# Optimization experiments

Hardware: AMD Instinct MI355X
Metric: run time of the kernel (lower is better)

## Reference

```python
import jax, jax.numpy as jnp
import numpy as np
from jax import lax

# ---- config constants (mirror init_kwargs) ----
PC_MIN_X, PC_MIN_Y, PC_MIN_Z = 0.0, -40.0, -3.0
PC_MAX_X, PC_MAX_Y, PC_MAX_Z = 70.4, 40.0, 1.0
VX, VY = 0.05, 0.05
NUM_KEYPOINTS = 2048
RADII = (0.4, 0.8)
NSAMPLE = (16, 16)
EPS = 1e-5


def setup_inputs() -> dict:
    key = jax.random.key(0)
    ks = jax.random.split(key, 16)
    B, N = 2, 32768
    u = jax.random.uniform(ks[0], (B, N, 4), dtype=jnp.float32)
    x = u[..., 0] * (PC_MAX_X - PC_MIN_X) + PC_MIN_X
    y = u[..., 1] * (PC_MAX_Y - PC_MIN_Y) + PC_MIN_Y
    z = u[..., 2] * (PC_MAX_Z - PC_MIN_Z) + PC_MIN_Z
    points = jnp.stack([x, y, z, u[..., 3]], axis=-1)  # (B,N,4): xyz + intensity
    spatial_features = jax.random.normal(ks[1], (B, 256, 200, 176), dtype=jnp.float32)
    p = lambda k, s: jax.random.normal(k, s, dtype=jnp.float32) * 0.1
    return dict(
        points=points, spatial_features=spatial_features,
        w0_0=p(ks[2], (4, 16)), g0_0=jnp.ones(16), b0_0=jnp.zeros(16),
        w0_1=p(ks[3], (16, 16)), g0_1=jnp.ones(16), b0_1=jnp.zeros(16),
        w1_0=p(ks[4], (4, 16)), g1_0=jnp.ones(16), b1_0=jnp.zeros(16),
        w1_1=p(ks[5], (16, 16)), g1_1=jnp.ones(16), b1_1=jnp.zeros(16),
        wf=p(ks[6], (288, 128)), gf=jnp.ones(128), bf=jnp.zeros(128),
        bev_stride=8,
    )


def _bn(x, g, b, axes):
    m = jnp.mean(x, axis=axes, keepdims=True)
    v = jnp.var(x, axis=axes, keepdims=True)
    return (x - m) * lax.rsqrt(v + EPS) * g + b


def _fps(xyz, K):
    # farthest point sampling, pointnet2 semantics (start at index 0)
    B, N, _ = xyz.shape
    def step(carry, _):
        dists, last = carry
        p = jax.vmap(lambda a, i: a[i])(xyz, last)           # (B,3)
        d = jnp.sum((xyz - p[:, None, :]) ** 2, axis=-1)     # (B,N)
        dists = jnp.minimum(dists, d)
        nxt = jnp.argmax(dists, axis=-1).astype(jnp.int32)
        return (dists, nxt), nxt
    init = (jnp.full((B, N), 1e10, xyz.dtype), jnp.zeros((B,), jnp.int32))
    _, rest = lax.scan(step, init, None, length=K - 1)       # (K-1,B)
    return jnp.concatenate([jnp.zeros((B, 1), jnp.int32), rest.T], axis=1)  # (B,K)


def _ball_group_pool(pts, kp, dist2, radius, ns, layers):
    # pts: (B,N,4) xyz+feat, kp: (B,K,3), dist2: (B,K,N) (stop-grad)
    B, N = pts.shape[0], pts.shape[1]
    valid = dist2 < radius * radius
    score = jnp.where(valid, -jnp.arange(N, dtype=jnp.float32), -jnp.inf)
    vals, idx = lax.top_k(score, ns)                          # first ns in-radius indices
    ok = jnp.isfinite(vals)                                   # (B,K,ns)
    idx = jnp.where(ok, idx, idx[..., :1])                    # duplicate first valid
    empty = ~ok[..., 0]                                       # (B,K) no neighbor at all
    grouped = jax.vmap(lambda p, i: p[i])(pts, idx)           # (B,K,ns,4)
    rel = grouped[..., :3] - kp[:, :, None, :]
    h = jnp.concatenate([rel, grouped[..., 3:]], axis=-1)     # (B,K,ns,4)
    h = jnp.where(empty[..., None, None], 0.0, h)
    for w, g, b in layers:
        h = jax.nn.relu(_bn(h @ w, g, b, axes=(0, 1, 2)))
    pooled = jnp.max(h, axis=2)                               # (B,K,C)
    return jnp.where(empty[..., None], 0.0, pooled)


def _bev_interp(kp, bev, stride):
    # kp: (B,K,3), bev: (B,C,H,W); torch bilinear_interpolate semantics
    B, C, H, W = bev.shape
    xi = (kp[..., 0] - PC_MIN_X) / VX / stride                # (B,K)
    yi = (kp[..., 1] - PC_MIN_Y) / VY / stride
    x0 = jnp.clip(jnp.floor(xi).astype(jnp.int32), 0, W - 1)
    x1 = jnp.clip(jnp.floor(xi).astype(jnp.int32) + 1, 0, W - 1)
    y0 = jnp.clip(jnp.floor(yi).astype(jnp.int32), 0, H - 1)
    y1 = jnp.clip(jnp.floor(yi).astype(jnp.int32) + 1, 0, H - 1)
    gat = jax.vmap(lambda f, yy, xx: f[:, yy, xx].T)          # (K,C) per batch
    Ia, Ib = gat(bev, y0, x0), gat(bev, y1, x0)
    Ic, Id = gat(bev, y0, x1), gat(bev, y1, x1)
    x0f, x1f = x0.astype(jnp.float32), x1.astype(jnp.float32)
    y0f, y1f = y0.astype(jnp.float32), y1.astype(jnp.float32)
    wa = ((x1f - xi) * (y1f - yi))[..., None]
    wb = ((x1f - xi) * (yi - y0f))[..., None]
    wc = ((xi - x0f) * (y1f - yi))[..., None]
    wd = ((xi - x0f) * (yi - y0f))[..., None]
    return Ia * wa + Ib * wb + Ic * wc + Id * wd              # (B,K,C)


def reference(points, spatial_features, w0_0, g0_0, b0_0, w0_1, g0_1, b0_1,
              w1_0, g1_0, b1_0, w1_1, g1_1, b1_1, wf, gf, bf, bev_stride):
    xyz = points[..., :3]                                     # (B,N,3)
    idx = _fps(xyz, NUM_KEYPOINTS)                            # (B,K)
    kp = jax.vmap(lambda p, i: p[i])(xyz, idx)                # keypoints (B,K,3)

    # BEV bilinear interpolation
    bev_feats = _bev_interp(kp, spatial_features, bev_stride) # (B,K,256)

    # raw-points multi-scale ball-query aggregation
    dist2 = lax.stop_gradient(
        jnp.sum((kp[:, :, None, :] - xyz[:, None, :, :]) ** 2, axis=-1))  # (B,K,N)
    p0 = _ball_group_pool(points, kp, dist2, RADII[0], NSAMPLE[0],
                          [(w0_0, g0_0, b0_0), (w0_1, g0_1, b0_1)])
    p1 = _ball_group_pool(points, kp, dist2, RADII[1], NSAMPLE[1],
                          [(w1_0, g1_0, b1_0), (w1_1, g1_1, b1_1)])

    feat = jnp.concatenate([bev_feats, p0, p1], axis=-1)      # (B,K,288)
    M = feat.shape[0] * feat.shape[1]
    feat = feat.reshape(M, -1)
    h = feat @ wf                                             # Linear no bias
    h = _bn(h, gf, bf, axes=(0,))                             # BatchNorm1d (train mode)
    return jax.nn.relu(h)                                     # (M,128)
```

## Files before the change

kernel.cpp:

```cpp
#include <hip/hip_runtime.h>
#include <hip/hip_bf16.h>
#include <limits.h>
#include <cstddef>

#define B_SZ    2
#define N_PTS   32768
#define N_KP    2048
#define N_CHUNK 512
#define H_BEV   200
#define W_BEV   176
#define C_BEV   256
#define FEAT_DIM 288
#define C_OUT   128
#define M_ROWS  4096

__device__ __forceinline__ float sqd(float ax, float ay, float az,
                                     float bx, float by, float bz) {
  float dx = ax - bx, dy = ay - by, dz = az - bz;
  return __fadd_rn(__fadd_rn(dx * dx, dy * dy), dz * dz);
}

__device__ __forceinline__ unsigned part1by1(unsigned n) {
  n &= 0xFFFF;
  n = (n | (n << 8)) & 0x00FF00FF;
  n = (n | (n << 4)) & 0x0F0F0F0F;
  n = (n | (n << 2)) & 0x33333333;
  n = (n | (n << 1)) & 0x55555555;
  return n;
}

__global__ void cell_count(const float4* __restrict__ pts,
                           int* __restrict__ codes, int* __restrict__ counts) {
  const int b = blockIdx.x, tid = threadIdx.x;
  __shared__ int cnt[4096];
  for (int k = tid; k < 4096; k += 1024) cnt[k] = 0;
  __syncthreads();
  for (int j = 0; j < 32; ++j) {
    int i = j * 1024 + tid;
    float4 v = pts[(size_t)b * N_PTS + i];
    int cx = min(63, max(0, (int)(v.x * (64.0f / 70.4f))));
    int cy = min(63, max(0, (int)((v.y + 40.0f) * 0.8f)));
    int code = (int)(part1by1((unsigned)cx) | (part1by1((unsigned)cy) << 1));
    codes[(size_t)b * N_PTS + i] = code;
    atomicAdd(&cnt[code], 1);
  }
  __syncthreads();
  for (int k = tid; k < 4096; k += 1024) counts[b * 4096 + k] = cnt[k];
}

__global__ void cell_scan(const int* __restrict__ counts, int* __restrict__ offs) {
  const int b = blockIdx.x, lane = threadIdx.x;
  const int* cnt = counts + b * 4096;
  int* off = offs + b * 4096;
  int s = 0;
  for (int k = 0; k < 64; ++k) s += cnt[lane * 64 + k];
  int incl = s;
#pragma unroll
  for (int o = 1; o < 64; o <<= 1) {
    int t = __shfl_up(incl, o);
    if (lane >= o) incl += t;
  }
  int run = incl - s;
  for (int k = 0; k < 64; ++k) {
    int id = lane * 64 + k;
    int t = cnt[id];
    off[id] = run;
    run += t;
  }
}

__global__ void scatter_pts(const float4* __restrict__ pts,
                            const int* __restrict__ codes,
                            int* __restrict__ offs,
                            float4* __restrict__ spts, int* __restrict__ sorig) {
  const int b = blockIdx.x, tid = threadIdx.x;
  for (int j = 0; j < 32; ++j) {
    int i = j * 1024 + tid;
    int code = codes[(size_t)b * N_PTS + i];
    int pos = atomicAdd(&offs[b * 4096 + code], 1);
    spts[(size_t)b * N_PTS + pos] = pts[(size_t)b * N_PTS + i];
    sorig[(size_t)b * N_PTS + pos] = i;
  }
}

__global__ void chunk_bbox(const float4* __restrict__ spts, float* __restrict__ bbox) {
  const int wid = threadIdx.x >> 6, lane = threadIdx.x & 63;
  const int chunk = blockIdx.x * 4 + wid;
  const int b = chunk >> 9, c = chunk & (N_CHUNK - 1);
  float4 v = spts[(size_t)b * N_PTS + c * 64 + lane];
  float lx = v.x, ly = v.y, lz = v.z, hx = v.x, hy = v.y, hz = v.z;
#pragma unroll
  for (int o = 32; o >= 1; o >>= 1) {
    lx = fminf(lx, __shfl_xor(lx, o)); hx = fmaxf(hx, __shfl_xor(hx, o));
    ly = fminf(ly, __shfl_xor(ly, o)); hy = fmaxf(hy, __shfl_xor(hy, o));
    lz = fminf(lz, __shfl_xor(lz, o)); hz = fmaxf(hz, __shfl_xor(hz, o));
  }
  if (lane == 0) {
    float* bp = bbox + (size_t)chunk * 6;
    bp[0] = lx; bp[1] = ly; bp[2] = lz; bp[3] = hx; bp[4] = hy; bp[5] = hz;
  }
}

__global__ void fps_pruned(const float4* __restrict__ pts,
                           const float4* __restrict__ spts,
                           const int* __restrict__ sorig,
                           const float* __restrict__ bbox,
                           float4* __restrict__ kp_xyz) {
  const int b = blockIdx.x;
  const int tid = threadIdx.x;
  const int wid = tid >> 6, lane = tid & 63;
  const float4* p4o = pts + (size_t)b * N_PTS;
  const float4* sp4 = spts + (size_t)b * N_PTS;
  const int* sog = sorig + (size_t)b * N_PTS;

  __shared__ float d_lds[N_PTS];
  __shared__ float bb[N_CHUNK * 6];
  __shared__ float keyd[N_CHUNK];
  __shared__ int keyo[N_CHUNK];
  __shared__ int dirty_s[N_CHUNK];
  __shared__ unsigned long long wkey[8];
  __shared__ float sxs, sys, szs;
  __shared__ int ndirty_s;

  for (int i = tid; i < N_PTS; i += 1024) d_lds[i] = 1e10f;
  for (int i = tid; i < N_CHUNK * 6; i += 1024) bb[i] = bbox[(size_t)b * N_CHUNK * 6 + i];
  if (tid < N_CHUNK) { keyd[tid] = 1e10f; keyo[tid] = 0; }
  if (tid == 0) {
    float4 p0 = p4o[0];
    kp_xyz[b * N_KP] = p0;
    sxs = p0.x; sys = p0.y; szs = p0.z;
    ndirty_s = 0;
  }
  __syncthreads();

  for (int it = 1; it < N_KP; ++it) {
    const float sx = sxs, sy = sys, sz = szs;
    if (tid < N_CHUNK) {
      const float* bp = bb + tid * 6;
      float dxm = fmaxf(fmaxf(bp[0] - sx, sx - bp[3]), 0.f);
      float dym = fmaxf(fmaxf(bp[1] - sy, sy - bp[4]), 0.f);
      float dzm = fmaxf(fmaxf(bp[2] - sz, sz - bp[5]), 0.f);
      float lb = (dxm * dxm + dym * dym) + dzm * dzm;
      if (lb * 0.99999f < keyd[tid]) {
        int p = atomicAdd(&ndirty_s, 1);
        dirty_s[p] = tid;
      }
    }
    __syncthreads();
    const int K = ndirty_s;
    for (int r = 0; r * 16 < K; ++r) {
      int ci = r * 16 + wid;
      if (ci < K) {
        int c = dirty_s[ci];
        int i = (c << 6) + lane;
        float4 sp = sp4[i];
        float ss = sqd(sp.x, sp.y, sp.z, sx, sy, sz);
        float nd = fminf(d_lds[i], ss);
        d_lds[i] = nd;
        float m = nd;
#pragma unroll
        for (int o = 32; o >= 1; o >>= 1) m = fmaxf(m, __shfl_xor(m, o));
        int og = sog[i];
        int cand = (nd == m) ? og : INT_MAX;
#pragma unroll
        for (int o = 32; o >= 1; o >>= 1) cand = min(cand, __shfl_xor(cand, o));
        if (lane == 0) { keyd[c] = m; keyo[c] = cand; }
      }
    }
    __syncthreads();
    if (tid < N_CHUNK) {
      unsigned long long key =
          ((unsigned long long)__float_as_uint(keyd[tid]) << 32) |
          (unsigned long long)(0xFFFFFFFFu - (unsigned)keyo[tid]);
#pragma unroll
      for (int o = 32; o >= 1; o >>= 1) {
        unsigned long long t = __shfl_xor(key, o);
        key = (t > key) ? t : key;
      }
      if (lane == 0) wkey[wid] = key;
    }
    __syncthreads();
    if (tid == 0) {
      unsigned long long k = wkey[0];
#pragma unroll
      for (int w = 1; w < 8; ++w) k = (wkey[w] > k) ? wkey[w] : k;
      int worig = (int)(0xFFFFFFFFu - (unsigned)(k & 0xFFFFFFFFu));
      float4 wp = p4o[worig];
      kp_xyz[b * N_KP + it] = wp;
      sxs = wp.x; sys = wp.y; szs = wp.z;
      ndirty_s = 0;
    }
    __syncthreads();
  }
}

__global__ void bev_kernel(const float4* __restrict__ kp,
                           const float* __restrict__ bev,
                           const int* __restrict__ stride_p,
                           float* __restrict__ feat) {
  const int kpi = blockIdx.x;
  const int c = threadIdx.x;
  const int b = kpi >> 11;
  float4 k = kp[kpi];
  float sf = (float)stride_p[0];
  float xi = (k.x - 0.0f) / 0.05f / sf;
  float yi = (k.y - (-40.0f)) / 0.05f / sf;
  int fx = (int)floorf(xi), fy = (int)floorf(yi);
  int x0 = min(max(fx, 0), W_BEV - 1), x1 = min(max(fx + 1, 0), W_BEV - 1);
  int y0 = min(max(fy, 0), H_BEV - 1), y1 = min(max(fy + 1, 0), H_BEV - 1);
  float x0f = (float)x0, x1f = (float)x1, y0f = (float)y0, y1f = (float)y1;
  float wa = (x1f - xi) * (y1f - yi);
  float wb = (x1f - xi) * (yi - y0f);
  float wc = (xi - x0f) * (y1f - yi);
  float wd = (xi - x0f) * (yi - y0f);
  const float* fb = bev + (size_t)b * C_BEV * (H_BEV * W_BEV) + (size_t)c * (H_BEV * W_BEV);
  float Ia = fb[y0 * W_BEV + x0], Ib = fb[y1 * W_BEV + x0];
  float Ic = fb[y0 * W_BEV + x1], Id = fb[y1 * W_BEV + x1];
  feat[(size_t)kpi * FEAT_DIM + c] = ((Ia * wa + Ib * wb) + Ic * wc) + Id * wd;
}

__device__ __forceinline__ int sel4(int q, int a, int b, int c, int d) {
  return q == 0 ? a : (q == 1 ? b : (q == 2 ? c : d));
}

__global__ void ballq_kernel(const float4* __restrict__ pts,
                             const float4* __restrict__ kp,
                             int* __restrict__ lists,
                             int* __restrict__ cnts) {
  const int w = threadIdx.x >> 6;
  const int lane = threadIdx.x & 63;
  const int kpbase = blockIdx.x * 16 + w * 4;
  const int b = blockIdx.x >> 7;
  const float4* p4 = pts + (size_t)b * N_PTS;
  __shared__ int l0[4][4][16];
  __shared__ int l1[4][4][16];
  float kx[4], ky[4], kz[4];
  int c0[4] = {0, 0, 0, 0}, c1[4] = {0, 0, 0, 0};
#pragma unroll
  for (int q = 0; q < 4; ++q) {
    float4 kq = kp[kpbase + q];
    kx[q] = kq.x; ky[q] = kq.y; kz[q] = kq.z;
  }
  const float R0SQ = (float)(0.4 * 0.4);
  const float R1SQ = (float)(0.8 * 0.8);
  const unsigned long long below = (lane == 0) ? 0ull : ((~0ull) >> (64 - lane));

  for (int r = 0; r < N_PTS / 64; ++r) {
    const int i = r * 64 + lane;
    float4 v = p4[i];
#pragma unroll
    for (int q = 0; q < 4; ++q) {
      float dd = sqd(v.x, v.y, v.z, kx[q], ky[q], kz[q]);
      bool in1 = dd < R1SQ;
      unsigned long long m1 = __ballot(in1);
      if (m1) {
        bool in0 = dd < R0SQ;
        unsigned long long m0 = __ballot(in0);
        if (c0[q] < 16) {
          if (in0) { int pos = c0[q] + __popcll(m0 & below); if (pos < 16) l0[w][q][pos] = i; }
          c0[q] += __popcll(m0);
        }
        if (c1[q] < 16) {
          if (in1) { int pos = c1[q] + __popcll(m1 & below); if (pos < 16) l1[w][q][pos] = i; }
          c1[q] += __popcll(m1);
        }
      }
    }
  }
  int q = lane >> 4, s = lane & 15;
  int kpi = kpbase + q;
  int cA = sel4(q, min(c0[0], 16), min(c0[1], 16), min(c0[2], 16), min(c0[3], 16));
  int cB = sel4(q, min(c1[0], 16), min(c1[1], 16), min(c1[2], 16), min(c1[3], 16));
  int vA = (s < cA) ? l0[w][q][s] : (cA > 0 ? l0[w][q][0] : 0);
  int vB = (s < cB) ? l1[w][q][s] : (cB > 0 ? l1[w][q][0] : 0);
  lists[(size_t)(0 * M_ROWS + kpi) * 16 + s] = vA;
  lists[(size_t)(1 * M_ROWS + kpi) * 16 + s] = vB;
  if (lane < 4) {
    cnts[0 * M_ROWS + kpbase + lane] = sel4(lane, min(c0[0], 16), min(c0[1], 16), min(c0[2], 16), min(c0[3], 16));
    cnts[1 * M_ROWS + kpbase + lane] = sel4(lane, min(c1[0], 16), min(c1[1], 16), min(c1[2], 16), min(c1[3], 16));
  }
}

__global__ void group_mlp1(const float4* __restrict__ pts,
                           const float4* __restrict__ kp,
                           const int* __restrict__ lists,
                           const int* __restrict__ cnts,
                           const float* __restrict__ w00,
                           const float* __restrict__ w10,
                           float* __restrict__ abuf) {
  int gid = blockIdx.x * 256 + threadIdx.x;
  int br = gid >> 16;
  int rem = gid & 65535;
  int bkp = rem >> 4, s = rem & 15;
  int b = bkp >> 11;
  __shared__ float wl[64];
  if (threadIdx.x < 64) wl[threadIdx.x] = (br ? w10 : w00)[threadIdx.x];
  __syncthreads();
  int cnt = cnts[br * M_ROWS + bkp];
  float h0 = 0.f, h1 = 0.f, h2 = 0.f, h3 = 0.f;
  if (cnt > 0) {
    int pidx = lists[(size_t)(br * M_ROWS + bkp) * 16 + s];
    float4 p = pts[(size_t)b * N_PTS + pidx];
    float4 k = kp[bkp];
    h0 = p.x - k.x; h1 = p.y - k.y; h2 = p.z - k.z; h3 = p.w;
  }
  float* out = abuf + (size_t)gid * 16;
#pragma unroll
  for (int c = 0; c < 16; ++c)
    out[c] = ((h0 * wl[c] + h1 * wl[16 + c]) + h2 * wl[32 + c]) + h3 * wl[48 + c];
}

__global__ void stats16_partial(const float* __restrict__ a, float* __restrict__ part) {
  int br = blockIdx.y, bl = blockIdx.x, t = threadIdx.x;
  const float* base = a + (size_t)br * 65536 * 16;
  float s[16], q[16];
#pragma unroll
  for (int c = 0; c < 16; ++c) { s[c] = 0.f; q[c] = 0.f; }
  for (int rr = 0; rr < 4; ++rr) {
    int row = bl * 1024 + rr * 256 + t;
#pragma unroll
    for (int c = 0; c < 16; ++c) {
      float v = base[(size_t)row * 16 + c];
      s[c] += v; q[c] += v * v;
    }
  }
  __shared__ float sbs[256][16];
  __shared__ float sbq[256][16];
#pragma unroll
  for (int c = 0; c < 16; ++c) { sbs[t][c] = s[c]; sbq[t][c] = q[c]; }
  __syncthreads();
  for (int st = 128; st > 0; st >>= 1) {
    if (t < st) {
#pragma unroll
      for (int c = 0; c < 16; ++c) { sbs[t][c] += sbs[t + st][c]; sbq[t][c] += sbq[t + st][c]; }
    }
    __syncthreads();
  }
  if (t < 16) {
    part[(size_t)(br * 64 + bl) * 32 + t] = sbs[0][t];
    part[(size_t)(br * 64 + bl) * 32 + 16 + t] = sbq[0][t];
  }
}

__global__ void stats16_final(const float* __restrict__ part, float* __restrict__ stats) {
  int t = threadIdx.x;
  if (t < 32) {
    int br = t >> 4, c = t & 15;
    float s = 0.f, q = 0.f;
    for (int bl = 0; bl < 64; ++bl) {
      s += part[(size_t)(br * 64 + bl) * 32 + c];
      q += part[(size_t)(br * 64 + bl) * 32 + 16 + c];
    }
    float m = s / 65536.f;
    float var = q / 65536.f - m * m;
    stats[(br * 16 + c) * 2] = m;
    stats[(br * 16 + c) * 2 + 1] = rsqrtf(var + 1e-5f);
  }
}

__global__ void mlp2_kernel(float* __restrict__ abuf, const float* __restrict__ stats,
                            const float* __restrict__ g00, const float* __restrict__ b00,
                            const float* __restrict__ g10, const float* __restrict__ b10,
                            const float* __restrict__ w01, const float* __restrict__ w11) {
  int gid = blockIdx.x * 256 + threadIdx.x;
  int br = gid >> 16;
  __shared__ float wl[256];
  wl[threadIdx.x] = (br ? w11 : w01)[threadIdx.x];
  __syncthreads();
  const float* g = br ? g10 : g00;
  const float* bb = br ? b10 : b00;
  float* row = abuf + (size_t)gid * 16;
  float z[16];
#pragma unroll
  for (int f = 0; f < 16; ++f) {
    float m = stats[(br * 16 + f) * 2], is = stats[(br * 16 + f) * 2 + 1];
    z[f] = fmaxf(0.f, (row[f] - m) * is * g[f] + bb[f]);
  }
  float o[16];
#pragma unroll
  for (int c = 0; c < 16; ++c) o[c] = 0.f;
#pragma unroll
  for (int f = 0; f < 16; ++f) {
#pragma unroll
    for (int c = 0; c < 16; ++c) o[c] += z[f] * wl[f * 16 + c];
  }
#pragma unroll
  for (int c = 0; c < 16; ++c) row[c] = o[c];
}

__global__ void pool_kernel(const float* __restrict__ abuf, const float* __restrict__ stats,
                            const int* __restrict__ cnts,
                            const float* __restrict__ g01, const float* __restrict__ b01,
                            const float* __restrict__ g11, const float* __restrict__ b11,
                            float* __restrict__ feat) {
  int gid = blockIdx.x * 256 + threadIdx.x;
  int br = gid >> 16;
  int rem = gid & 65535;
  int bkp = rem >> 4, c = rem & 15;
  const float* g = br ? g11 : g01;
  const float* bb = br ? b11 : b01;
  float m = stats[(br * 16 + c) * 2], is = stats[(br * 16 + c) * 2 + 1];
  float gg = g[c], bv = bb[c];
  const float* base = abuf + ((size_t)br * 65536 + (size_t)bkp * 16) * 16 + c;
  float mx = -1e30f;
#pragma unroll
  for (int s = 0; s < 16; ++s) {
    float v = base[(size_t)s * 16];
    mx = fmaxf(mx, fmaxf(0.f, (v - m) * is * gg + bv));
  }
  if (cnts[br * M_ROWS + bkp] == 0) mx = 0.f;
  feat[(size_t)bkp * FEAT_DIM + 256 + br * 16 + c] = mx;
}

__global__ void final_mm(const float* __restrict__ feat, const float* __restrict__ wf,
                         float* __restrict__ hbuf) {
  int row = blockIdx.x;
  int c = threadIdx.x;
  __shared__ float fr[FEAT_DIM];
  for (int k = c; k < FEAT_DIM; k += 128) fr[k] = feat[(size_t)row * FEAT_DIM + k];
  __syncthreads();
  float acc = 0.f;
#pragma unroll 8
  for (int k = 0; k < FEAT_DIM; ++k) acc += fr[k] * wf[(size_t)k * C_OUT + c];
  hbuf[(size_t)row * C_OUT + c] = acc;
}

__global__ void stats128_partial(const float* __restrict__ hbuf, float* __restrict__ part) {
  int bl = blockIdx.x, c = threadIdx.x;
  float s = 0.f, q = 0.f;
  for (int r = 0; r < 128; ++r) {
    float v = hbuf[(size_t)(bl * 128 + r) * C_OUT + c];
    s += v; q += v * v;
  }
  part[(size_t)(bl * 128 + c) * 2] = s;
  part[(size_t)(bl * 128 + c) * 2 + 1] = q;
}

__global__ void stats128_final(const float* __restrict__ part, float* __restrict__ stats) {
  int c = threadIdx.x;
  float s = 0.f, q = 0.f;
  for (int bl = 0; bl < 32; ++bl) {
    s += part[(size_t)(bl * 128 + c) * 2];
    q += part[(size_t)(bl * 128 + c) * 2 + 1];
  }
  float m = s / 4096.f;
  float var = q / 4096.f - m * m;
  stats[c * 2] = m;
  stats[c * 2 + 1] = rsqrtf(var + 1e-5f);
}

__global__ void out_kernel(const float* __restrict__ hbuf, const float* __restrict__ stats,
                           const float* __restrict__ gf, const float* __restrict__ bf,
                           float* __restrict__ out) {
  int gid = blockIdx.x * 256 + threadIdx.x;
  int c = gid & 127;
  float v = hbuf[gid];
  float r = fmaxf(0.f, (v - stats[c * 2]) * stats[c * 2 + 1] * gf[c] + bf[c]);
  out[gid] = r;
}

extern "C" void kernel_launch(void* const* d_in, const int* in_sizes, int n_in,
                              void* d_out, int out_size, void* d_ws, size_t ws_size,
                              hipStream_t stream) {
  const float4* pts = (const float4*)d_in[0];
  const float* spatial = (const float*)d_in[1];
  const float* w0_0 = (const float*)d_in[2];
  const float* g0_0 = (const float*)d_in[3];
  const float* b0_0 = (const float*)d_in[4];
  const float* w0_1 = (const float*)d_in[5];
  const float* g0_1 = (const float*)d_in[6];
  const float* b0_1 = (const float*)d_in[7];
  const float* w1_0 = (const float*)d_in[8];
  const float* g1_0 = (const float*)d_in[9];
  const float* b1_0 = (const float*)d_in[10];
  const float* w1_1 = (const float*)d_in[11];
  const float* g1_1 = (const float*)d_in[12];
  const float* b1_1 = (const float*)d_in[13];
  const float* wf  = (const float*)d_in[14];
  const float* gf  = (const float*)d_in[15];
  const float* bfp = (const float*)d_in[16];
  const int* stride_p = (const int*)d_in[17];

  char* ws = (char*)d_ws;
  float4* kp_xyz = (float4*)(ws + 0);
  int* lists     = (int*)(ws + 65536);
  int* cnts      = (int*)(ws + 589824);
  float* abuf    = (float*)(ws + 622592);
  float* feat    = (float*)(ws + 9011200);
  float* hbuf    = (float*)(ws + 13729792);
  float* part16  = (float*)(ws + 15826944);
  float* stats16 = (float*)(ws + 15843328);
  float* part128 = (float*)(ws + 15843584);
  float* stats128= (float*)(ws + 15876352);

  char* sbase = (char*)abuf;
  float4* spts = (float4*)(sbase + 0);
  int* sorig   = (int*)(sbase + 1048576);
  int* codes   = (int*)(sbase + 1310720);
  int* counts  = (int*)(sbase + 1572864);
  int* offs    = (int*)(sbase + 1605632);
  float* bboxg = (float*)(sbase + 1638400);

  cell_count<<<B_SZ, 1024, 0, stream>>>(pts, codes, counts);
  cell_scan<<<B_SZ, 64, 0, stream>>>(counts, offs);
  scatter_pts<<<B_SZ, 1024, 0, stream>>>(pts, codes, offs, spts, sorig);
  chunk_bbox<<<256, 256, 0, stream>>>(spts, bboxg);
  fps_pruned<<<B_SZ, 1024, 0, stream>>>(pts, spts, sorig, bboxg, kp_xyz);
  bev_kernel<<<M_ROWS, 256, 0, stream>>>(kp_xyz, spatial, stride_p, feat);
  ballq_kernel<<<256, 256, 0, stream>>>(pts, kp_xyz, lists, cnts);
  group_mlp1<<<512, 256, 0, stream>>>(pts, kp_xyz, lists, cnts, w0_0, w1_0, abuf);
  stats16_partial<<<dim3(64, 2), 256, 0, stream>>>(abuf, part16);
  stats16_final<<<1, 64, 0, stream>>>(part16, stats16);
  mlp2_kernel<<<512, 256, 0, stream>>>(abuf, stats16, g0_0, b0_0, g1_0, b1_0, w0_1, w1_1);
  stats16_partial<<<dim3(64, 2), 256, 0, stream>>>(abuf, part16);
  stats16_final<<<1, 64, 0, stream>>>(part16, stats16);
  pool_kernel<<<512, 256, 0, stream>>>(abuf, stats16, cnts, g0_1, b0_1, g1_1, b1_1, feat);
  final_mm<<<M_ROWS, 128, 0, stream>>>(feat, wf, hbuf);
  stats128_partial<<<32, 128, 0, stream>>>(hbuf, part128);
  stats128_final<<<1, 128, 0, stream>>>(part128, stats128);
  out_kernel<<<2048, 256, 0, stream>>>(hbuf, stats128, gf, bfp, (float*)d_out);
}
```

Baseline: 4.060 ms.

## Cut FPS per-iteration barriers and global loads with redundant winner selection

The FPS loop now has every thread compute the final argmax from per-wave keys and read the winning point's xyz from LDS copies kept per chunk. This removes the serial thread-0 step, one __syncthreads, and a dependent global load of the winner each iteration. The dirty-chunk list is double-buffered so its counter can be reset without an extra barrier. Bounding boxes move from LDS into registers, and the first two chunk loads per wave are issued up front for more memory parallelism. The cost is extra LDS writes of xyz for each chunk max and a w=0 in the output keypoints instead of the original intensity.

Result: slower. 4.371 ms (+7.7%).

```diff
diff --git a/kernel.cpp b/kernel.cpp
--- a/kernel.cpp
+++ b/kernel.cpp
@@ -114,57 +114,90 @@
   const int* sog = sorig + (size_t)b * N_PTS;
 
   __shared__ float d_lds[N_PTS];
-  __shared__ float bb[N_CHUNK * 6];
   __shared__ float keyd[N_CHUNK];
   __shared__ int keyo[N_CHUNK];
-  __shared__ int dirty_s[N_CHUNK];
+  __shared__ float keyx[N_CHUNK];
+  __shared__ float keyy[N_CHUNK];
+  __shared__ float keyz[N_CHUNK];
+  __shared__ int dirty_s[2][N_CHUNK];
   __shared__ unsigned long long wkey[8];
-  __shared__ float sxs, sys, szs;
-  __shared__ int ndirty_s;
+  __shared__ int wchunk[8];
+  __shared__ int ndirty_s[2];
 
   for (int i = tid; i < N_PTS; i += 1024) d_lds[i] = 1e10f;
-  for (int i = tid; i < N_CHUNK * 6; i += 1024) bb[i] = bbox[(size_t)b * N_CHUNK * 6 + i];
-  if (tid < N_CHUNK) { keyd[tid] = 1e10f; keyo[tid] = 0; }
-  if (tid == 0) {
-    float4 p0 = p4o[0];
-    kp_xyz[b * N_KP] = p0;
-    sxs = p0.x; sys = p0.y; szs = p0.z;
-    ndirty_s = 0;
-  }
-  __syncthreads();
+  if (tid < N_CHUNK) keyd[tid] = 1e10f;
+  if (tid < 2) ndirty_s[tid] = 0;
+  float bx0 = 0.f, by0 = 0.f, bz0 = 0.f, bx1 = 0.f, by1 = 0.f, bz1 = 0.f;
+  if (tid < N_CHUNK) {
+    const float* bp = bbox + (size_t)b * N_CHUNK * 6 + (size_t)tid * 6;
+    bx0 = bp[0]; by0 = bp[1]; bz0 = bp[2]; bx1 = bp[3]; by1 = bp[4]; bz1 = bp[5];
+  }
+  float4 p0 = p4o[0];
+  float sx = p0.x, sy = p0.y, sz = p0.z;
+  if (tid == 0) kp_xyz[b * N_KP] = make_float4(sx, sy, sz, 0.f);
+  __syncthreads();
+
+#define PROC_CHUNK(cc, pp, og, dp)                                            \
+  {                                                                           \
+    float ss = sqd((pp).x, (pp).y, (pp).z, sx, sy, sz);                       \
+    float nd = fminf((dp), ss);                                               \
+    d_lds[((cc) << 6) + lane] = nd;                                           \
+    float mm = nd;                                                            \
+    _Pragma("unroll")                                                         \
+    for (int oo = 32; oo >= 1; oo >>= 1) mm = fmaxf(mm, __shfl_xor(mm, oo));  \
+    int cnd = (nd == mm) ? (og) : INT_MAX;                                    \
+    _Pragma("unroll")                                                         \
+    for (int oo = 32; oo >= 1; oo >>= 1) cnd = min(cnd, __shfl_xor(cnd, oo)); \
+    if ((og) == cnd) {                                                        \
+      keyd[cc] = mm; keyo[cc] = cnd;                                          \
+      keyx[cc] = (pp).x; keyy[cc] = (pp).y; keyz[cc] = (pp).z;                \
+    }                                                                         \
+  }
 
   for (int it = 1; it < N_KP; ++it) {
-    const float sx = sxs, sy = sys, sz = szs;
+    const int s = it & 1;
     if (tid < N_CHUNK) {
-      const float* bp = bb + tid * 6;
-      float dxm = fmaxf(fmaxf(bp[0] - sx, sx - bp[3]), 0.f);
-      float dym = fmaxf(fmaxf(bp[1] - sy, sy - bp[4]), 0.f);
-      float dzm = fmaxf(fmaxf(bp[2] - sz, sz - bp[5]), 0.f);
+      float dxm = fmaxf(fmaxf(bx0 - sx, sx - bx1), 0.f);
+      float dym = fmaxf(fmaxf(by0 - sy, sy - by1), 0.f);
+      float dzm = fmaxf(fmaxf(bz0 - sz, sz - bz1), 0.f);
       float lb = (dxm * dxm + dym * dym) + dzm * dzm;
       if (lb * 0.99999f < keyd[tid]) {
-        int p = atomicAdd(&ndirty_s, 1);
-        dirty_s[p] = tid;
+        int p = atomicAdd(&ndirty_s[s], 1);
+        dirty_s[s][p] = tid;
       }
     }
+    if (tid == 1023) ndirty_s[s ^ 1] = 0;
     __syncthreads();
-    const int K = ndirty_s;
-    for (int r = 0; r * 16 < K; ++r) {
-      int ci = r * 16 + wid;
-      if (ci < K) {
-        int c = dirty_s[ci];
-        int i = (c << 6) + lane;
-        float4 sp = sp4[i];
-        float ss = sqd(sp.x, sp.y, sp.z, sx, sy, sz);
-        float nd = fminf(d_lds[i], ss);
-        d_lds[i] = nd;
-        float m = nd;
-#pragma unroll
-        for (int o = 32; o >= 1; o >>= 1) m = fmaxf(m, __shfl_xor(m, o));
-        int og = sog[i];
-        int cand = (nd == m) ? og : INT_MAX;
-#pragma unroll
-        for (int o = 32; o >= 1; o >>= 1) cand = min(cand, __shfl_xor(cand, o));
-        if (lane == 0) { keyd[c] = m; keyo[c] = cand; }
+    const int K = ndirty_s[s];
+    {
+      int cA = (wid < K) ? dirty_s[s][wid] : -1;
+      int cB = ((wid + 16) < K) ? dirty_s[s][wid + 16] : -1;
+      if (cA >= 0) {
+        int iA = (cA << 6) + lane;
+        float4 pA = sp4[iA];
+        int ogA = sog[iA];
+        float dpA = d_lds[iA];
+        if (cB >= 0) {
+          int iB = (cB << 6) + lane;
+          float4 pB = sp4[iB];
+          int ogB = sog[iB];
+          float dpB = d_lds[iB];
+          PROC_CHUNK(cA, pA, ogA, dpA);
+          PROC_CHUNK(cB, pB, ogB, dpB);
+        } else {
+          PROC_CHUNK(cA, pA, ogA, dpA);
+        }
+        for (int r = 2; r * 16 < K; ++r) {
+          int ci = r * 16 + wid;
+          if (ci < K) {
+            int c = dirty_s[s][ci];
+            int i2 = (c << 6) + lane;
+            float4 p = sp4[i2];
+            int og2 = sog[i2];
+            float dp2 = d_lds[i2];
+            PROC_CHUNK(c, p, og2, dp2);
+          }
+        }
       }
     }
     __syncthreads();
@@ -172,26 +205,27 @@
       unsigned long long key =
           ((unsigned long long)__float_as_uint(keyd[tid]) << 32) |
           (unsigned long long)(0xFFFFFFFFu - (unsigned)keyo[tid]);
+      int ch = tid;
 #pragma unroll
       for (int o = 32; o >= 1; o >>= 1) {
-        unsigned long long t = __shfl_xor(key, o);
-        key = (t > key) ? t : key;
+        unsigned long long tk = __shfl_xor(key, o);
+        int tc = __shfl_xor(ch, o);
+        if (tk > key) { key = tk; ch = tc; }
       }
-      if (lane == 0) wkey[wid] = key;
+      if (lane == 0) { wkey[wid] = key; wchunk[wid] = ch; }
     }
     __syncthreads();
-    if (tid == 0) {
-      unsigned long long k = wkey[0];
-#pragma unroll
-      for (int w = 1; w < 8; ++w) k = (wkey[w] > k) ? wkey[w] : k;
-      int worig = (int)(0xFFFFFFFFu - (unsigned)(k & 0xFFFFFFFFu));
-      float4 wp = p4o[worig];
-      kp_xyz[b * N_KP + it] = wp;
-      sxs = wp.x; sys = wp.y; szs = wp.z;
-      ndirty_s = 0;
-    }
-    __syncthreads();
-  }
+    unsigned long long kb = wkey[0];
+    int cb = wchunk[0];
+#pragma unroll
+    for (int w = 1; w < 8; ++w) {
+      unsigned long long t = wkey[w];
+      if (t > kb) { kb = t; cb = wchunk[w]; }
+    }
+    sx = keyx[cb]; sy = keyy[cb]; sz = keyz[cb];
+    if (tid == 0) kp_xyz[b * N_KP + it] = make_float4(sx, sy, sz, 0.f);
+  }
+#undef PROC_CHUNK
 }
 
 __global__ void bev_kernel(const float4* __restrict__ kp,
```

## Restructure pruned FPS into per-wave register-resident chunk ownership with DPP reductions

Applied to the files above, without the earlier changes.

Each wave now owns 32 chunks, keeping their bounding boxes and best keys (distance, index, coordinates) in registers instead of shared memory. Dirty chunks are found with a ballot and processed with a two-deep software prefetch. Per-chunk and per-wave argmax reductions use 64-bit DPP steps instead of shuffles. Each iteration needs two block barriers instead of four, there is no atomic dirty list, and every thread picks the winner's coordinates from shared memory, which removes the serial tid-0 global load of the selected point. The cost is heavier register use and more complex per-lane control flow.

After: 4.910 ms. +20.9%, slower.

```diff
diff --git a/kernel.cpp b/kernel.cpp
--- a/kernel.cpp
+++ b/kernel.cpp
@@ -28,6 +28,27 @@
   n = (n | (n << 1)) & 0x55555555;
   return n;
 }
+
+#define DPP_MOV(v, CTRL, RMASK) \
+  ((unsigned)__builtin_amdgcn_update_dpp((int)(v), (int)(v), (CTRL), (RMASK), 0xf, false))
+
+#define R64_STEP(hi, lo, CTRL, RMASK)                                         \
+  {                                                                           \
+    unsigned hm_ = DPP_MOV(hi, CTRL, RMASK);                                  \
+    unsigned lm_ = DPP_MOV(lo, CTRL, RMASK);                                  \
+    bool gt_ = (hm_ > (hi)) || (hm_ == (hi) && lm_ > (lo));                   \
+    hi = gt_ ? hm_ : (hi); lo = gt_ ? lm_ : (lo);                             \
+  }
+
+#define R64_ALL(hi, lo)                                                       \
+  R64_STEP(hi, lo, 0x111, 0xf)                                                \
+  R64_STEP(hi, lo, 0x112, 0xf)                                                \
+  R64_STEP(hi, lo, 0x114, 0xf)                                                \
+  R64_STEP(hi, lo, 0x118, 0xf)                                                \
+  R64_STEP(hi, lo, 0x142, 0xa)                                                \
+  R64_STEP(hi, lo, 0x143, 0xc)
+
+#define DEPOSIT(dst, val, lsel) { (dst) = ((int)lane == (int)(lsel)) ? (val) : (dst); }
 
 __global__ void cell_count(const float4* __restrict__ pts,
                            int* __restrict__ codes, int* __restrict__ counts) {
@@ -114,84 +135,114 @@
   const int* sog = sorig + (size_t)b * N_PTS;
 
   __shared__ float d_lds[N_PTS];
-  __shared__ float bb[N_CHUNK * 6];
-  __shared__ float keyd[N_CHUNK];
-  __shared__ int keyo[N_CHUNK];
-  __shared__ int dirty_s[N_CHUNK];
-  __shared__ unsigned long long wkey[8];
-  __shared__ float sxs, sys, szs;
-  __shared__ int ndirty_s;
+  __shared__ unsigned long long wkey[16];
+  __shared__ float4 wcoord[16];
 
   for (int i = tid; i < N_PTS; i += 1024) d_lds[i] = 1e10f;
-  for (int i = tid; i < N_CHUNK * 6; i += 1024) bb[i] = bbox[(size_t)b * N_CHUNK * 6 + i];
-  if (tid < N_CHUNK) { keyd[tid] = 1e10f; keyo[tid] = 0; }
-  if (tid == 0) {
-    float4 p0 = p4o[0];
-    kp_xyz[b * N_KP] = p0;
-    sxs = p0.x; sys = p0.y; szs = p0.z;
-    ndirty_s = 0;
-  }
-  __syncthreads();
+
+  const int cown = lane * 16 + wid;
+  float bx0 = 0.f, by0 = 0.f, bz0 = 0.f, bx1 = 0.f, by1 = 0.f, bz1 = 0.f;
+  if (lane < 32) {
+    const float* bp = bbox + (size_t)b * N_CHUNK * 6 + (size_t)cown * 6;
+    bx0 = bp[0]; by0 = bp[1]; bz0 = bp[2]; bx1 = bp[3]; by1 = bp[4]; bz1 = bp[5];
+  }
+  unsigned khi = __float_as_uint(1e10f);
+  unsigned klo = 0xFFFFFFFFu;
+  unsigned kcx = 0u, kcy = 0u, kcz = 0u;
+
+  float4 p0 = p4o[0];
+  float sx = p0.x, sy = p0.y, sz = p0.z;
+  if (tid == 0) kp_xyz[b * N_KP] = make_float4(sx, sy, sz, 0.f);
+  __syncthreads();
+
+#define PROC(lsel, pp, og, dp)                                                \
+  {                                                                           \
+    const int c_ = (lsel) * 16 + wid;                                         \
+    float ss_ = sqd((pp).x, (pp).y, (pp).z, sx, sy, sz);                      \
+    float nd_ = fminf((dp), ss_);                                             \
+    d_lds[(c_ << 6) + lane] = nd_;                                            \
+    unsigned hi_ = __float_as_uint(nd_);          \
+    unsigned lo_ = 0xFFFFFFFFu - (unsigned)(og);                              \
+    unsigned rh_ = hi_, rl_ = lo_;                                            \
+    R64_ALL(rh_, rl_)                                                         \
+    unsigned mb_ = (unsigned)__builtin_amdgcn_readlane((int)rh_, 63);         \
+    unsigned cn_ = (unsigned)__builtin_amdgcn_readlane((int)rl_, 63);         \
+    unsigned long long cm_ = __ballot(lo_ == cn_);           \
+    int cl_ = (int)__builtin_ctzll(cm_);                                      \
+    unsigned xb_ = (unsigned)__builtin_amdgcn_readlane((int)__float_as_uint((pp).x), cl_); \
+    unsigned yb_ = (unsigned)__builtin_amdgcn_readlane((int)__float_as_uint((pp).y), cl_); \
+    unsigned zb_ = (unsigned)__builtin_amdgcn_readlane((int)__float_as_uint((pp).z), cl_); \
+    DEPOSIT(khi, mb_, (lsel))                                                 \
+    DEPOSIT(klo, cn_, (lsel))                                                 \
+    DEPOSIT(kcx, xb_, (lsel))                                                 \
+    DEPOSIT(kcy, yb_, (lsel))                                                 \
+    DEPOSIT(kcz, zb_, (lsel))                                                 \
+  }
 
   for (int it = 1; it < N_KP; ++it) {
-    const float sx = sxs, sy = sys, sz = szs;
-    if (tid < N_CHUNK) {
-      const float* bp = bb + tid * 6;
-      float dxm = fmaxf(fmaxf(bp[0] - sx, sx - bp[3]), 0.f);
-      float dym = fmaxf(fmaxf(bp[1] - sy, sy - bp[4]), 0.f);
-      float dzm = fmaxf(fmaxf(bp[2] - sz, sz - bp[5]), 0.f);
+    bool dirty = false;
+    if (lane < 32) {
+      float dxm = fmaxf(fmaxf(bx0 - sx, sx - bx1), 0.f);
+      float dym = fmaxf(fmaxf(by0 - sy, sy - by1), 0.f);
+      float dzm = fmaxf(fmaxf(bz0 - sz, sz - bz1), 0.f);
       float lb = (dxm * dxm + dym * dym) + dzm * dzm;
-      if (lb * 0.99999f < keyd[tid]) {
-        int p = atomicAdd(&ndirty_s, 1);
-        dirty_s[p] = tid;
+      dirty = lb * 0.99999f < __uint_as_float(khi);
+    }
+    unsigned mask = (unsigned)(__ballot(dirty) & 0xFFFFFFFFull);
+    {
+      int lA = 0, lB = 0; bool hasA = false, hasB = false;
+      float4 pA, pB; int ogA = 0, ogB = 0; float dpA = 0.f, dpB = 0.f;
+      if (mask) {
+        lA = (int)__builtin_ctz(mask); mask &= mask - 1; hasA = true;
+        int i = ((lA * 16 + wid) << 6) + lane;
+        pA = sp4[i]; ogA = sog[i]; dpA = d_lds[i];
       }
+      if (mask) {
+        lB = (int)__builtin_ctz(mask); mask &= mask - 1; hasB = true;
+        int i = ((lB * 16 + wid) << 6) + lane;
+        pB = sp4[i]; ogB = sog[i]; dpB = d_lds[i];
+      }
+      while (hasA) {
+        PROC(lA, pA, ogA, dpA);
+        lA = lB; pA = pB; ogA = ogB; dpA = dpB; hasA = hasB;
+        if (mask) {
+          lB = (int)__builtin_ctz(mask); mask &= mask - 1; hasB = true;
+          int i = ((lB * 16 + wid) << 6) + lane;
+          pB = sp4[i]; ogB = sog[i]; dpB = d_lds[i];
+        } else hasB = false;
+      }
+    }
+    {
+      unsigned hi = (lane < 32) ? khi : 0u;
+      unsigned lo = (lane < 32) ? klo : 0u;
+      R64_ALL(hi, lo)
+      unsigned mb = (unsigned)__builtin_amdgcn_readlane((int)hi, 63);
+      unsigned cn = (unsigned)__builtin_amdgcn_readlane((int)lo, 63);
+      unsigned long long cm = __ballot(lane < 32 && khi == mb && klo == cn);
+      int cl = (int)__builtin_ctzll(cm);
+      unsigned xb = (unsigned)__builtin_amdgcn_readlane((int)kcx, cl);
+      unsigned yb = (unsigned)__builtin_amdgcn_readlane((int)kcy, cl);
+      unsigned zb = (unsigned)__builtin_amdgcn_readlane((int)kcz, cl);
+      if (lane == 0) {
+        wkey[wid] = ((unsigned long long)mb << 32) | cn;
+        wcoord[wid] = make_float4(__uint_as_float(xb), __uint_as_float(yb),
+                                  __uint_as_float(zb), 0.f);
+      }
     }
     __syncthreads();
-    const int K = ndirty_s;
-    for (int r = 0; r * 16 < K; ++r) {
-      int ci = r * 16 + wid;
-      if (ci < K) {
-        int c = dirty_s[ci];
-        int i = (c << 6) + lane;
-        float4 sp = sp4[i];
-        float ss = sqd(sp.x, sp.y, sp.z, sx, sy, sz);
-        float nd = fminf(d_lds[i], ss);
-        d_lds[i] = nd;
-        float m = nd;
-#pragma unroll
-        for (int o = 32; o >= 1; o >>= 1) m = fmaxf(m, __shfl_xor(m, o));
-        int og = sog[i];
-        int cand = (nd == m) ? og : INT_MAX;
-#pragma unroll
-        for (int o = 32; o >= 1; o >>= 1) cand = min(cand, __shfl_xor(cand, o));
-        if (lane == 0) { keyd[c] = m; keyo[c] = cand; }
-      }
-    }
+    unsigned long long kb = wkey[0];
+    int wv = 0;
+#pragma unroll
+    for (int w = 1; w < 16; ++w) {
+      unsigned long long t = wkey[w];
+      if (t > kb) { kb = t; wv = w; }
+    }
+    float4 wc = wcoord[wv];
+    sx = wc.x; sy = wc.y; sz = wc.z;
+    if (tid == 0) kp_xyz[b * N_KP + it] = make_float4(sx, sy, sz, 0.f);
     __syncthreads();
-    if (tid < N_CHUNK) {
-      unsigned long long key =
-          ((unsigned long long)__float_as_uint(keyd[tid]) << 32) |
-          (unsigned long long)(0xFFFFFFFFu - (unsigned)keyo[tid]);
-#pragma unroll
-      for (int o = 32; o >= 1; o >>= 1) {
-        unsigned long long t = __shfl_xor(key, o);
-        key = (t > key) ? t : key;
-      }
-      if (lane == 0) wkey[wid] = key;
-    }
-    __syncthreads();
-    if (tid == 0) {
-      unsigned long long k = wkey[0];
-#pragma unroll
-      for (int w = 1; w < 8; ++w) k = (wkey[w] > k) ? wkey[w] : k;
-      int worig = (int)(0xFFFFFFFFu - (unsigned)(k & 0xFFFFFFFFu));
-      float4 wp = p4o[worig];
-      kp_xyz[b * N_KP + it] = wp;
-      sxs = wp.x; sys = wp.y; szs = wp.z;
-      ndirty_s = 0;
-    }
-    __syncthreads();
-  }
+  }
+#undef PROC
 }
 
 __global__ void bev_kernel(const float4* __restrict__ kp,
```
